# Optimization experiments

Hardware: AMD Instinct MI355X
Metric: run time of the kernel (lower is better)

Reference implementation:

```python
import jax, jax.numpy as jnp
import numpy as np

B, T, HD = 256, 512, 256
NREAL, NCAT, NCLS, ESZ = 8, 4, 10, 8
FEAT = NREAL + NCAT * NCLS          # 48 input feature dim
EMB = NREAL + NCAT * ESZ            # 40 = sum(embedding_size)
NEG_SLOPE = 0.1


def setup_inputs():
    key = jax.random.key(0)
    ks = jax.random.split(key, 18)
    g = lambda i, shape: (jax.random.normal(ks[i], shape, jnp.float32) * 0.05)
    return dict(
        x0=jax.random.normal(ks[0], (B, T, FEAT), jnp.float32),
        emb_w=g(1, (NCAT, NCLS, ESZ)),
        w1=g(2, (EMB, HD)), b1=g(3, (HD,)),
        w2=g(4, (HD, HD)), b2=g(5, (HD,)),
        wi_f=g(6, (HD, 4 * HD)), bi_f=g(7, (4 * HD,)),
        wh_f=g(8, (HD, 4 * HD)), bh_f=g(9, (4 * HD,)),
        wi_r=g(10, (HD, 4 * HD)), bi_r=g(11, (4 * HD,)),
        wh_r=g(12, (HD, 4 * HD)), bh_r=g(13, (4 * HD,)),
        w3=g(14, (2 * HD, 1)), b3=g(15, (1,)),
    )


def _lstm_final(x, wi, bi, wh, bh):
    # x: [B, T, H] -> final hidden state [B, H]; gate order F, I, A, O.
    h = wh.shape[0]
    gx = jnp.einsum('bth,hg->tbg', x, wi) + bi  # precompute i2h for all steps
    q0 = jnp.zeros((x.shape[0], h), x.dtype)
    s0 = jnp.zeros((x.shape[0], h), x.dtype)

    def step(carry, g_t):
        q, s = carry
        gates = g_t + q @ wh + bh
        f, i, a, o = jnp.split(gates, 4, axis=-1)
        s = jax.nn.sigmoid(f) * s + jax.nn.sigmoid(i) * jnp.tanh(a)
        q = jax.nn.sigmoid(o) * jnp.tanh(s)
        return (q, s), None

    (q, _), _ = jax.lax.scan(step, (q0, s0), gx)
    return q


def reference(x0, emb_w, w1, b1, w2, b2,
              wi_f, bi_f, wh_f, bh_f, wi_r, bi_r, wh_r, bh_r, w3, b3):
    lrelu = lambda v: jnp.where(v >= 0, v, NEG_SLOPE * v)
    b, t = x0.shape[0], x0.shape[1]
    x_real = x0[..., :NREAL]
    # soft embedding of categorical one-hot blocks: [B,T,NCAT,NCLS] @ [NCAT,NCLS,ESZ]
    x_cat = x0[..., NREAL:].reshape(b, t, NCAT, NCLS)
    x_emb = jnp.einsum('btcn,cne->btce', x_cat, emb_w).reshape(b, t, NCAT * ESZ)
    x1 = jnp.concatenate([x_real, x_emb], axis=-1)
    x2 = lrelu(x1 @ w1 + b1)
    x3 = lrelu(x2 @ w2 + b2)
    q_f = _lstm_final(x3, wi_f, bi_f, wh_f, bh_f)
    q_r = _lstm_final(x3[:, ::-1, :], wi_r, bi_r, wh_r, bh_r)
    x4 = jnp.concatenate([q_f, q_r], axis=1)
    return x4 @ w3 + b3
```

## Files before the change

### kernel.cpp

```cpp
#include <hip/hip_runtime.h>


#define DI __device__ __forceinline__
typedef unsigned short u16;
typedef __attribute__((ext_vector_type(8))) __bf16 bf16x8;
typedef __attribute__((ext_vector_type(8))) short short8;
typedef __attribute__((ext_vector_type(4))) float f32x4;
typedef __attribute__((ext_vector_type(2))) unsigned int u32x2;

DI float bf2f(u16 u){ unsigned v = ((unsigned)u)<<16; float f; __builtin_memcpy(&f,&v,4); return f; }
DI u16 f2bf(float f){ unsigned u; __builtin_memcpy(&u,&f,4);
  unsigned r = (u + 0x7fffu + ((u>>16)&1u))>>16; return (u16)r; }
DI float sigf(float x){ return __builtin_amdgcn_rcpf(1.f + __builtin_amdgcn_exp2f(-1.44269504f*x)); }
DI float tanh_(float x){ return 1.f - 2.f*__builtin_amdgcn_rcpf(1.f + __builtin_amdgcn_exp2f(2.88539008f*x)); }

DI void gl_lds16(const void* g, void* lds){
  __builtin_amdgcn_global_load_lds(
    (const __attribute__((address_space(1))) unsigned int*)g,
    (__attribute__((address_space(3))) unsigned int*)lds,
    16, 0, 0);
}
DI bf16x8 ld8(const void* p){ return *(const bf16x8*)p; }

__global__ void disc_wsfail(float* out){ out[0] = 1.0e9f; }

__global__ __launch_bounds__(256) void disc_prep(
    const float* __restrict__ embw, const float* __restrict__ w1, const float* __restrict__ w2,
    const float* __restrict__ wi_f, const float* __restrict__ wi_r,
    const float* __restrict__ wh_f, const float* __restrict__ wh_r,
    const float* __restrict__ bi_f, const float* __restrict__ bh_f,
    const float* __restrict__ bi_r, const float* __restrict__ bh_r,
    u16* __restrict__ w1effT, u16* __restrict__ w2bT, u16* __restrict__ wibT,
    u16* __restrict__ whp, float* __restrict__ biasf)
{
  int bx = blockIdx.x, tid = threadIdx.x;
  if (bx < 64) {
    int i = bx*256 + tid; int n = i>>6, f = i&63;
    float v = 0.f;
    if (f < 8) v = w1[f*256 + n];
    else if (f < 48) {
      int ff = f-8, c = ff/10, cls = ff%10;
      #pragma unroll
      for (int e=0;e<8;e++) v += embw[(c*10+cls)*8 + e] * w1[(8 + c*8 + e)*256 + n];
    }
    w1effT[n*64 + f] = f2bf(v);
  } else if (bx < 320) {
    int i = (bx-64)*256 + tid; int n = i>>8, k = i&255;
    w2bT[i] = f2bf(w2[k*256 + n]);
  } else if (bx < 2368) {
    int i = (bx-320)*256 + tid; int n = i>>8, k = i&255;
    const float* wi = (n < 1024) ? wi_f : wi_r; int g = n & 1023;
    wibT[i] = f2bf(wi[k*1024 + g]);
  } else if (bx < 4416) {
    int i = (bx-2368)*256 + tid;
    int j = i&7, lane = (i>>3)&63, nt = (i>>9)&7, kt = (i>>12)&7, w = (i>>15)&7, dir = (i>>18)&1;
    int k = kt*32 + (lane>>4)*8 + j;
    int g = (nt>>1)*256 + w*32 + (nt&1)*16 + (lane&15);
    const float* wh = dir ? wh_r : wh_f;
    whp[i] = f2bf(wh[k*1024 + g]);
  } else {
    int i = (bx-4416)*256 + tid;
    if (i < 2048) { int dir = i>>10, g = i&1023;
      biasf[i] = dir ? (bi_r[g]+bh_r[g]) : (bi_f[g]+bh_f[g]); }
  }
}

__global__ __launch_bounds__(256) void disc_k1a(const float* __restrict__ x0,
    const u16* __restrict__ w1effT, const float* __restrict__ b1, u16* __restrict__ x2)
{
  __shared__ __align__(16) u16 a_lds[64*64];
  __shared__ __align__(16) u16 b_lds[256*64];
  int tid=threadIdx.x, lane=tid&63, wv=tid>>6;
  int m0 = blockIdx.x*64;
  #pragma unroll
  for (int r2=0;r2<8;r2++){
    int c = r2*256 + tid;
    gl_lds16((const char*)w1effT + (size_t)c*16, (char*)b_lds + (r2*256 + wv*64)*16);
  }
  if (tid < 128){
    int row = tid>>1, half = tid&1;
    const float* src = x0 + (size_t)(m0+row)*48 + half*24;
    u16 tmp[24];
    #pragma unroll
    for (int i=0;i<24;i++) tmp[i] = f2bf(src[i]);
    #pragma unroll
    for (int i=0;i<3;i++) *(short8*)&a_lds[row*64 + half*24 + i*8] = *(short8*)&tmp[i*8];
    if (half){ short8 z = (short8){0,0,0,0,0,0,0,0};
      *(short8*)&a_lds[row*64 + 48] = z; *(short8*)&a_lds[row*64 + 56] = z; }
  }
  asm volatile("s_waitcnt vmcnt(0)" ::: "memory");
  __syncthreads();
  bf16x8 Af0 = ld8(&a_lds[(wv*16 + (lane&15))*64 + (lane>>4)*8]);
  bf16x8 Af1 = ld8(&a_lds[(wv*16 + (lane&15))*64 + 32 + (lane>>4)*8]);
  f32x4 acc[16];
  #pragma unroll
  for (int ni=0;ni<16;ni++){
    acc[ni] = (f32x4){0.f,0.f,0.f,0.f};
    bf16x8 B0 = ld8(&b_lds[(ni*16 + (lane&15))*64 + (lane>>4)*8]);
    bf16x8 B1 = ld8(&b_lds[(ni*16 + (lane&15))*64 + 32 + (lane>>4)*8]);
    acc[ni] = __builtin_amdgcn_mfma_f32_16x16x32_bf16(Af0, B0, acc[ni], 0,0,0);
    acc[ni] = __builtin_amdgcn_mfma_f32_16x16x32_bf16(Af1, B1, acc[ni], 0,0,0);
  }
  #pragma unroll
  for (int ni=0;ni<16;ni++){
    float bb = b1[ni*16 + (lane&15)];
    #pragma unroll
    for (int r=0;r<4;r++){
      float v = acc[ni][r] + bb; v = v>=0.f ? v : 0.1f*v;
      int row = m0 + wv*16 + (lane>>4)*4 + r;
      x2[(size_t)row*256 + ni*16 + (lane&15)] = f2bf(v);
    }
  }
}

__global__ __launch_bounds__(256) void disc_k1b(const u16* __restrict__ x2,
    const u16* __restrict__ w2bT, const float* __restrict__ b2, u16* __restrict__ x3t)
{
  __shared__ __align__(16) u16 a_lds[64*64];
  __shared__ __align__(16) u16 b_lds[256*64];
  int tid=threadIdx.x, lane=tid&63, wv=tid>>6;
  int m0 = blockIdx.x*64;
  f32x4 acc[16];
  #pragma unroll
  for (int ni=0;ni<16;ni++) acc[ni] = (f32x4){0.f,0.f,0.f,0.f};
  for (int kt=0;kt<4;kt++){
    #pragma unroll
    for (int r2=0;r2<2;r2++){
      int c = r2*256 + tid, row = c>>3, cb = (c&7)*16;
      gl_lds16((const char*)x2 + (size_t)(m0+row)*512 + kt*128 + cb,
               (char*)a_lds + (r2*256 + wv*64)*16);
    }
    #pragma unroll
    for (int r2=0;r2<8;r2++){
      int c = r2*256 + tid, row = c>>3, cb = (c&7)*16;
      gl_lds16((const char*)w2bT + (size_t)row*512 + kt*128 + cb,
               (char*)b_lds + (r2*256 + wv*64)*16);
    }
    asm volatile("s_waitcnt vmcnt(0)" ::: "memory");
    __syncthreads();
    bf16x8 Af0 = ld8(&a_lds[(wv*16 + (lane&15))*64 + (lane>>4)*8]);
    bf16x8 Af1 = ld8(&a_lds[(wv*16 + (lane&15))*64 + 32 + (lane>>4)*8]);
    #pragma unroll
    for (int ni=0;ni<16;ni++){
      bf16x8 B0 = ld8(&b_lds[(ni*16 + (lane&15))*64 + (lane>>4)*8]);
      bf16x8 B1 = ld8(&b_lds[(ni*16 + (lane&15))*64 + 32 + (lane>>4)*8]);
      acc[ni] = __builtin_amdgcn_mfma_f32_16x16x32_bf16(Af0, B0, acc[ni], 0,0,0);
      acc[ni] = __builtin_amdgcn_mfma_f32_16x16x32_bf16(Af1, B1, acc[ni], 0,0,0);
    }
    __syncthreads();
  }
  #pragma unroll
  for (int ni=0;ni<16;ni++){
    float bb = b2[ni*16 + (lane&15)];
    #pragma unroll
    for (int r=0;r<4;r++){
      float v = acc[ni][r] + bb; v = v>=0.f ? v : 0.1f*v;
      int rowg = m0 + wv*16 + (lane>>4)*4 + r;
      int b = rowg>>9, t = rowg&511;
      x3t[((size_t)t*256 + b)*256 + ni*16 + (lane&15)] = f2bf(v);
    }
  }
}

__global__ __launch_bounds__(256) void disc_k1c(const u16* __restrict__ x3t,
    const u16* __restrict__ wibT, const float* __restrict__ biasf,
    u16* __restrict__ gxc, int chunk)
{
  __shared__ __align__(16) u16 a_lds[128*64];
  __shared__ __align__(16) u16 b_lds[128*64];
  int tid=threadIdx.x, lane=tid&63, wv=tid>>6;
  int id = (blockIdx.x & 7)*256 + (blockIdx.x >> 3);
  int dirn = id >> 10;
  int rem  = id & 1023;
  int tloc = rem >> 4;
  int msub = (rem >> 3) & 1;
  int nt8  = rem & 7;
  int tp    = chunk*64 + tloc;
  int tglob = dirn ? (511 - tp) : tp;
  int m0 = tglob*256 + msub*128;
  int n0 = dirn*1024 + nt8*128;
  int wm = wv>>1, wn = wv&1;
  f32x4 acc[4][4];
  #pragma unroll
  for (int mi=0;mi<4;mi++)
    #pragma unroll
    for (int ni=0;ni<4;ni++) acc[mi][ni] = (f32x4){0.f,0.f,0.f,0.f};
  for (int kt=0;kt<4;kt++){
    #pragma unroll
    for (int r2=0;r2<4;r2++){
      int c = r2*256 + tid, row = c>>3, cb = (c&7)*16;
      gl_lds16((const char*)x3t + (size_t)(m0+row)*512 + kt*128 + cb,
               (char*)a_lds + (r2*256 + wv*64)*16);
    }
    #pragma unroll
    for (int r2=0;r2<4;r2++){
      int c = r2*256 + tid, row = c>>3, cb = (c&7)*16;
      gl_lds16((const char*)wibT + (size_t)(n0+row)*512 + kt*128 + cb,
               (char*)b_lds + (r2*256 + wv*64)*16);
    }
    asm volatile("s_waitcnt vmcnt(0)" ::: "memory");
    __syncthreads();
    bf16x8 Af[4][2], Bf[4][2];
    #pragma unroll
    for (int mi=0;mi<4;mi++){
      Af[mi][0] = ld8(&a_lds[(wm*64+mi*16+(lane&15))*64 + (lane>>4)*8]);
      Af[mi][1] = ld8(&a_lds[(wm*64+mi*16+(lane&15))*64 + 32 + (lane>>4)*8]);
    }
    #pragma unroll
    for (int ni=0;ni<4;ni++){
      Bf[ni][0] = ld8(&b_lds[(wn*64+ni*16+(lane&15))*64 + (lane>>4)*8]);
      Bf[ni][1] = ld8(&b_lds[(wn*64+ni*16+(lane&15))*64 + 32 + (lane>>4)*8]);
    }
    #pragma unroll
    for (int ks=0;ks<2;ks++)
      #pragma unroll
      for (int mi=0;mi<4;mi++)
        #pragma unroll
        for (int ni=0;ni<4;ni++)
          acc[mi][ni] = __builtin_amdgcn_mfma_f32_16x16x32_bf16(Af[mi][ks], Bf[ni][ks], acc[mi][ni], 0,0,0);
    __syncthreads();
  }
  float bb[4];
  #pragma unroll
  for (int ni=0;ni<4;ni++) bb[ni] = biasf[n0 + wn*64 + ni*16 + (lane&15)];
  #pragma unroll
  for (int mi=0;mi<4;mi++){
    int bbase = msub*128 + wm*64 + mi*16;
    #pragma unroll
    for (int ni=0;ni<4;ni++){
      int g0 = (n0 + wn*64 + ni*16) & 1023;
      int gt = g0>>8, h0 = g0&255;
      int w8 = h0>>5, p = (h0>>4)&1, nt = gt*2 + p;
      size_t fb = (((((size_t)tloc*2 + dirn)*16 + (bbase>>4))*8 + w8)*8 + nt)*256;
      u32x2 v;
      v.x = (unsigned)f2bf(acc[mi][ni][0]+bb[ni]) | ((unsigned)f2bf(acc[mi][ni][1]+bb[ni])<<16);
      v.y = (unsigned)f2bf(acc[mi][ni][2]+bb[ni]) | ((unsigned)f2bf(acc[mi][ni][3]+bb[ni])<<16);
      *(u32x2*)((char*)gxc + (fb + (size_t)lane*4)*2) = v;
    }
  }
}

__global__ __launch_bounds__(512) __attribute__((amdgpu_waves_per_eu(2, 2)))
void disc_k2(const u16* __restrict__ gxc, const u16* __restrict__ whp,
             u16* __restrict__ qsave, float* __restrict__ ssave,
             float* __restrict__ qout, int chunk)
{
  __shared__ __align__(16) u16 wh_lds[65536];
  __shared__ __align__(16) u16 qbuf0[4096];
  __shared__ __align__(16) u16 qbuf1[4096];
  int tid=threadIdx.x, lane=tid&63, w=tid>>6;
  int bid=blockIdx.x, dir=bid>>4, blk=bid&15;
  int tbase = chunk*64;
  int row = lane&15, rgrp = lane>>4;

  const char* whpw = (const char*)whp + (size_t)(dir*8+w)*65536;

  #pragma unroll
  for (int i=0;i<16;i++){
    int kt=i>>1, p=i&1;
    gl_lds16(whpw + (kt*8+5+p)*1024 + lane*16, (char*)wh_lds + (w*16 + i)*1024);
  }
  bf16x8 whr[8][5];
  #pragma unroll
  for (int kt=0;kt<8;kt++)
    #pragma unroll
    for (int nt=0;nt<5;nt++)
      whr[kt][nt] = ld8(whpw + (kt*8+nt)*1024 + lane*16);

  float sst[2][4];
  if (chunk==0){
    #pragma unroll
    for (int p=0;p<2;p++)
      #pragma unroll
      for (int r=0;r<4;r++) sst[p][r]=0.f;
    *(short8*)&qbuf0[tid*8] = (short8){0,0,0,0,0,0,0,0};
  } else {
    f32x4 s0 = *(const f32x4*)&ssave[((size_t)bid*512+tid)*8];
    f32x4 s1 = *(const f32x4*)&ssave[((size_t)bid*512+tid)*8 + 4];
    sst[0][0]=s0[0]; sst[0][1]=s0[1]; sst[0][2]=s0[2]; sst[0][3]=s0[3];
    sst[1][0]=s1[0]; sst[1][1]=s1[1]; sst[1][2]=s1[2]; sst[1][3]=s1[3];
    *(short8*)&qbuf0[tid*8] = *(const short8*)&qsave[(size_t)bid*4096 + tid*8];
  }

  int aoff[8];
  #pragma unroll
  for (int kt=0;kt<8;kt++)
    aoff[kt] = ((row)*512 + ((kt*64 + rgrp*16) ^ ((lane&7)<<4))) >> 1;
  int woff[2][4];
  #pragma unroll
  for (int p=0;p<2;p++)
    #pragma unroll
    for (int r=0;r<4;r++){
      int bb = rgrp*4 + r;
      woff[p][r] = (bb*512 + ((w*64 + p*32 + row*2) ^ ((bb&7)<<4))) >> 1;
    }
  int qoutbase = dir*65536 + blk*4096 + w*32 + row;
  const char* gxb = (const char*)gxc + ((size_t)(dir*16+blk)*8 + w)*4096 + (size_t)lane*8;

  asm volatile("s_waitcnt vmcnt(0)" ::: "memory");
  __syncthreads();

#define STEP(TL, QR, QW) { \
    const int tl = (TL); \
    const char* gp = gxb + (size_t)tl*1048576; \
    u32x2 gt[8]; \
    _Pragma("unroll") for (int nt=0;nt<8;nt++) gt[nt] = *(const u32x2*)(const void*)(gp + nt*512); \
    f32x4 acc[8]; \
    _Pragma("unroll") for (int nt=0;nt<8;nt++){ \
      acc[nt][0] = bf2f((u16)(gt[nt].x));       acc[nt][1] = bf2f((u16)(gt[nt].x >> 16)); \
      acc[nt][2] = bf2f((u16)(gt[nt].y));       acc[nt][3] = bf2f((u16)(gt[nt].y >> 16)); \
    } \
    bf16x8 Afr[2], sA[2]; \
    Afr[0] = ld8(&QR[aoff[0]]); \
    sA[0]  = ld8(whpw + (0*8+7)*1024 + lane*16); \
    _Pragma("unroll") for (int kt=0;kt<8;kt++){ \
      const int cur = kt&1, nxt = (kt+1)&1; \
      if (kt<7){ \
        Afr[nxt] = ld8(&QR[aoff[kt+1]]); \
        sA[nxt]  = ld8(whpw + ((kt+1)*8+7)*1024 + lane*16); \
      } \
      bf16x8 lA = ld8((char*)wh_lds + (w*16 + kt*2+0)*1024 + lane*16); \
      bf16x8 lB = ld8((char*)wh_lds + (w*16 + kt*2+1)*1024 + lane*16); \
      acc[0] = __builtin_amdgcn_mfma_f32_16x16x32_bf16(Afr[cur], whr[kt][0], acc[0], 0,0,0); \
      acc[1] = __builtin_amdgcn_mfma_f32_16x16x32_bf16(Afr[cur], whr[kt][1], acc[1], 0,0,0); \
      acc[2] = __builtin_amdgcn_mfma_f32_16x16x32_bf16(Afr[cur], whr[kt][2], acc[2], 0,0,0); \
      acc[3] = __builtin_amdgcn_mfma_f32_16x16x32_bf16(Afr[cur], whr[kt][3], acc[3], 0,0,0); \
      acc[4] = __builtin_amdgcn_mfma_f32_16x16x32_bf16(Afr[cur], whr[kt][4], acc[4], 0,0,0); \
      acc[5] = __builtin_amdgcn_mfma_f32_16x16x32_bf16(Afr[cur], lA,         acc[5], 0,0,0); \
      acc[6] = __builtin_amdgcn_mfma_f32_16x16x32_bf16(Afr[cur], lB,         acc[6], 0,0,0); \
      acc[7] = __builtin_amdgcn_mfma_f32_16x16x32_bf16(Afr[cur], sA[cur],    acc[7], 0,0,0); \
    } \
    float qv[2][4]; \
    _Pragma("unroll") for (int p=0;p<2;p++) \
      _Pragma("unroll") for (int r=0;r<4;r++){ \
        float fg = sigf (acc[0+p][r]); \
        float ig = sigf (acc[2+p][r]); \
        float ag = tanh_(acc[4+p][r]); \
        float og = sigf (acc[6+p][r]); \
        float s = fg*sst[p][r] + ig*ag; sst[p][r] = s; \
        qv[p][r] = og*tanh_(s); \
      } \
    if (tbase + tl == 511){ \
      _Pragma("unroll") for (int p=0;p<2;p++) \
        _Pragma("unroll") for (int r=0;r<4;r++) \
          qout[qoutbase + (rgrp*4 + r)*256 + p*16] = qv[p][r]; \
    } else { \
      _Pragma("unroll") for (int p=0;p<2;p++) \
        _Pragma("unroll") for (int r=0;r<4;r++) \
          QW[woff[p][r]] = f2bf(qv[p][r]); \
    } \
    __syncthreads(); \
  }

  for (int t2=0;t2<64;t2+=2){
    STEP(t2,   qbuf0, qbuf1)
    STEP(t2+1, qbuf1, qbuf0)
  }
#undef STEP

  if (chunk < 7){
    *(short8*)&qsave[(size_t)bid*4096 + tid*8] = *(const short8*)&qbuf0[tid*8];
    f32x4 s0 = (f32x4){sst[0][0],sst[0][1],sst[0][2],sst[0][3]};
    f32x4 s1 = (f32x4){sst[1][0],sst[1][1],sst[1][2],sst[1][3]};
    *(f32x4*)&ssave[((size_t)bid*512+tid)*8]     = s0;
    *(f32x4*)&ssave[((size_t)bid*512+tid)*8 + 4] = s1;
  }
}

__global__ __launch_bounds__(256) void disc_k3(const float* __restrict__ qout,
    const float* __restrict__ w3, const float* __restrict__ b3, float* __restrict__ out)
{
  int b = threadIdx.x;
  const float* qf = qout + (size_t)b*256;
  const float* qr = qout + 65536 + (size_t)b*256;
  float acc = b3[0];
  #pragma unroll 4
  for (int h=0;h<256;h++) acc += qf[h]*w3[h] + qr[h]*w3[256+h];
  out[b] = acc;
}

extern "C" void kernel_launch(void* const* d_in, const int* in_sizes, int n_in,
                              void* d_out, int out_size, void* d_ws, size_t ws_size,
                              hipStream_t stream)
{
  const float* x0   = (const float*)d_in[0];
  const float* embw = (const float*)d_in[1];
  const float* w1   = (const float*)d_in[2];
  const float* b1   = (const float*)d_in[3];
  const float* w2   = (const float*)d_in[4];
  const float* b2   = (const float*)d_in[5];
  const float* wi_f = (const float*)d_in[6];
  const float* bi_f = (const float*)d_in[7];
  const float* wh_f = (const float*)d_in[8];
  const float* bh_f = (const float*)d_in[9];
  const float* wi_r = (const float*)d_in[10];
  const float* bi_r = (const float*)d_in[11];
  const float* wh_r = (const float*)d_in[12];
  const float* bh_r = (const float*)d_in[13];
  const float* w3   = (const float*)d_in[14];
  const float* b3   = (const float*)d_in[15];

  const size_t NEED = 137797632ull;
  if (ws_size < NEED){
    disc_wsfail<<<dim3(1), dim3(1), 0, stream>>>((float*)d_out);
    return;
  }

  char* ws = (char*)d_ws;
  u16*   x2    = (u16*)  (ws);
  u16*   gxc   = (u16*)  (ws);
  u16*   x3t   = (u16*)  (ws + 67108864ull);
  u16*   whp   = (u16*)  (ws + 134217728ull);
  u16*   w1eT  = (u16*)  (ws + 135266304ull);
  u16*   w2bT  = (u16*)  (ws + 135299072ull);
  u16*   wibT  = (u16*)  (ws + 135430144ull);
  float* biasf = (float*)(ws + 136478720ull);
  float* qout  = (float*)(ws + 136486912ull);
  u16*   qsave = (u16*)  (ws + 137011200ull);
  float* ssave = (float*)(ws + 137273344ull);

  disc_prep<<<dim3(4424), dim3(256), 0, stream>>>(embw, w1, w2, wi_f, wi_r, wh_f, wh_r,
                                                  bi_f, bh_f, bi_r, bh_r,
                                                  w1eT, w2bT, wibT, whp, biasf);
  disc_k1a<<<dim3(2048), dim3(256), 0, stream>>>(x0, w1eT, b1, x2);
  disc_k1b<<<dim3(2048), dim3(256), 0, stream>>>(x2, w2bT, b2, x3t);
  for (int c = 0; c < 8; ++c){
    disc_k1c<<<dim3(2048), dim3(256), 0, stream>>>(x3t, wibT, biasf, gxc, c);
    disc_k2 <<<dim3(32),   dim3(512), 0, stream>>>(gxc, whp, qsave, ssave, qout, c);
  }
  disc_k3<<<dim3(1), dim3(256), 0, stream>>>(qout, w3, b3, (float*)d_out);
}
```

Baseline: 1.960 ms.

## Double-buffer per-step gate inputs in LDS and keep more recurrent weights in registers

The LSTM recurrence kernel now prefetches the next timestep's precomputed input-gate tile into a second LDS buffer with async global-to-LDS loads. The current step then reads its gate inputs from LDS, so global-load latency is taken off the serial per-step critical path. One more weight column tile is also moved from LDS into registers, which halves the LDS weight footprint and the per-kt LDS reads. In exchange, register pressure rises at two waves per EU, which risks spills. Correctness also relies on the barrier at the end of each step waiting for the outstanding async loads.

```diff
diff --git a/kernel.cpp b/kernel.cpp
--- a/kernel.cpp
+++ b/kernel.cpp
@@ -245,7 +245,8 @@
              u16* __restrict__ qsave, float* __restrict__ ssave,
              float* __restrict__ qout, int chunk)
 {
-  __shared__ __align__(16) u16 wh_lds[65536];
+  __shared__ __align__(16) u16 wh_lds[32768];
+  __shared__ __align__(16) u16 gx_lds[2][16384];
   __shared__ __align__(16) u16 qbuf0[4096];
   __shared__ __align__(16) u16 qbuf1[4096];
   int tid=threadIdx.x, lane=tid&63, w=tid>>6;
@@ -254,17 +255,20 @@
   int row = lane&15, rgrp = lane>>4;
 
   const char* whpw = (const char*)whp + (size_t)(dir*8+w)*65536;
-
-  #pragma unroll
-  for (int i=0;i<16;i++){
-    int kt=i>>1, p=i&1;
-    gl_lds16(whpw + (kt*8+5+p)*1024 + lane*16, (char*)wh_lds + (w*16 + i)*1024);
-  }
-  bf16x8 whr[8][5];
+  const char* gxsrc = (const char*)gxc + ((size_t)(dir*16)+blk)*32768;
+
+  #pragma unroll
+  for (int i=0;i<8;i++)
+    gl_lds16(whpw + (i*8+6)*1024 + lane*16, (char*)wh_lds + (w*8 + i)*1024);
+  #pragma unroll
+  for (int i=0;i<4;i++)
+    gl_lds16(gxsrc + w*4096 + i*1024 + lane*16,
+             (char*)gx_lds[0] + w*4096 + i*1024 + lane*16);
+  bf16x8 whr[8][6];
   #pragma unroll
   for (int kt=0;kt<8;kt++)
     #pragma unroll
-    for (int nt=0;nt<5;nt++)
+    for (int nt=0;nt<6;nt++)
       whr[kt][nt] = ld8(whpw + (kt*8+nt)*1024 + lane*16);
 
   float sst[2][4];
@@ -295,16 +299,20 @@
       woff[p][r] = (bb*512 + ((w*64 + p*32 + row*2) ^ ((bb&7)<<4))) >> 1;
     }
   int qoutbase = dir*65536 + blk*4096 + w*32 + row;
-  const char* gxb = (const char*)gxc + ((size_t)(dir*16+blk)*8 + w)*4096 + (size_t)lane*8;
 
   asm volatile("s_waitcnt vmcnt(0)" ::: "memory");
   __syncthreads();
 
-#define STEP(TL, QR, QW) { \
+#define STEP(TL, QR, QW, CUR) { \
     const int tl = (TL); \
-    const char* gp = gxb + (size_t)tl*1048576; \
+     \
+    if (tl < 63){ const char* gs = gxsrc + (size_t)(tl+1)*1048576 + w*4096; \
+      _Pragma("unroll") for (int i=0;i<4;i++) \
+        gl_lds16(gs + i*1024 + lane*16, (char*)gx_lds[(CUR)^1] + w*4096 + i*1024 + lane*16); } \
+     \
+    const char* glp = (const char*)gx_lds[CUR] + w*4096 + (size_t)lane*8; \
     u32x2 gt[8]; \
-    _Pragma("unroll") for (int nt=0;nt<8;nt++) gt[nt] = *(const u32x2*)(const void*)(gp + nt*512); \
+    _Pragma("unroll") for (int nt=0;nt<8;nt++) gt[nt] = *(const u32x2*)(const void*)(glp + nt*512); \
     f32x4 acc[8]; \
     _Pragma("unroll") for (int nt=0;nt<8;nt++){ \
       acc[nt][0] = bf2f((u16)(gt[nt].x));       acc[nt][1] = bf2f((u16)(gt[nt].x >> 16)); \
@@ -319,15 +327,14 @@
         Afr[nxt] = ld8(&QR[aoff[kt+1]]); \
         sA[nxt]  = ld8(whpw + ((kt+1)*8+7)*1024 + lane*16); \
       } \
-      bf16x8 lA = ld8((char*)wh_lds + (w*16 + kt*2+0)*1024 + lane*16); \
-      bf16x8 lB = ld8((char*)wh_lds + (w*16 + kt*2+1)*1024 + lane*16); \
+      bf16x8 lA = ld8((char*)wh_lds + (w*8 + kt)*1024 + lane*16); \
       acc[0] = __builtin_amdgcn_mfma_f32_16x16x32_bf16(Afr[cur], whr[kt][0], acc[0], 0,0,0); \
       acc[1] = __builtin_amdgcn_mfma_f32_16x16x32_bf16(Afr[cur], whr[kt][1], acc[1], 0,0,0); \
       acc[2] = __builtin_amdgcn_mfma_f32_16x16x32_bf16(Afr[cur], whr[kt][2], acc[2], 0,0,0); \
       acc[3] = __builtin_amdgcn_mfma_f32_16x16x32_bf16(Afr[cur], whr[kt][3], acc[3], 0,0,0); \
       acc[4] = __builtin_amdgcn_mfma_f32_16x16x32_bf16(Afr[cur], whr[kt][4], acc[4], 0,0,0); \
-      acc[5] = __builtin_amdgcn_mfma_f32_16x16x32_bf16(Afr[cur], lA,         acc[5], 0,0,0); \
-      acc[6] = __builtin_amdgcn_mfma_f32_16x16x32_bf16(Afr[cur], lB,         acc[6], 0,0,0); \
+      acc[5] = __builtin_amdgcn_mfma_f32_16x16x32_bf16(Afr[cur], whr[kt][5], acc[5], 0,0,0); \
+      acc[6] = __builtin_amdgcn_mfma_f32_16x16x32_bf16(Afr[cur], lA,         acc[6], 0,0,0); \
       acc[7] = __builtin_amdgcn_mfma_f32_16x16x32_bf16(Afr[cur], sA[cur],    acc[7], 0,0,0); \
     } \
     float qv[2][4]; \
@@ -353,8 +360,8 @@
   }
 
   for (int t2=0;t2<64;t2+=2){
-    STEP(t2,   qbuf0, qbuf1)
-    STEP(t2+1, qbuf1, qbuf0)
+    STEP(t2,   qbuf0, qbuf1, ((t2)&1))
+    STEP(t2+1, qbuf1, qbuf0, ((t2+1)&1))
   }
 #undef STEP
 
```

Measured after the change: 2.815 ms. +43.6%, slower.

## Overlap next-chunk input projection with LSTM recurrence in a fused launch

Applied to the files above, without the earlier changes.

Splits the time axis into 16 chunks of 32 steps and fuses the input-gate GEMM for chunk c+1 into the same launch as the recurrent LSTM for chunk c. Extra blocks beyond the first 32 compute the next chunk's gate pre-activations into a double-buffered workspace, while the first 32 blocks run the serial recurrence. The aim is to hide the GEMM behind the latency-bound recurrence, which uses only 32 CUs, and to avoid serialising separate kernels. In exchange the launch count doubles, the GEMM blocks carry the recurrent kernel's large LDS footprint and 512-thread shape, and the recurrent blocks may compete with them for CU resources.

```diff
diff --git a/kernel.cpp b/kernel.cpp
--- a/kernel.cpp
+++ b/kernel.cpp
@@ -169,13 +169,13 @@
   __shared__ __align__(16) u16 a_lds[128*64];
   __shared__ __align__(16) u16 b_lds[128*64];
   int tid=threadIdx.x, lane=tid&63, wv=tid>>6;
-  int id = (blockIdx.x & 7)*256 + (blockIdx.x >> 3);
-  int dirn = id >> 10;
-  int rem  = id & 1023;
+  int id = (blockIdx.x & 7)*128 + (blockIdx.x >> 3);
+  int dirn = id >> 9;
+  int rem  = id & 511;
   int tloc = rem >> 4;
   int msub = (rem >> 3) & 1;
   int nt8  = rem & 7;
-  int tp    = chunk*64 + tloc;
+  int tp    = chunk*32 + tloc;
   int tglob = dirn ? (511 - tp) : tp;
   int m0 = tglob*256 + msub*128;
   int n0 = dirn*1024 + nt8*128;
@@ -241,16 +241,93 @@
 }
 
 __global__ __launch_bounds__(512) __attribute__((amdgpu_waves_per_eu(2, 2)))
-void disc_k2(const u16* __restrict__ gxc, const u16* __restrict__ whp,
-             u16* __restrict__ qsave, float* __restrict__ ssave,
-             float* __restrict__ qout, int chunk)
+void disc_fused(const u16* __restrict__ gxr, u16* __restrict__ gxw,
+                const u16* __restrict__ whp,
+                const u16* __restrict__ x3t, const u16* __restrict__ wibT,
+                const float* __restrict__ biasf,
+                u16* __restrict__ qsave, float* __restrict__ ssave,
+                float* __restrict__ qout, int chunk)
 {
   __shared__ __align__(16) u16 wh_lds[65536];
   __shared__ __align__(16) u16 qbuf0[4096];
   __shared__ __align__(16) u16 qbuf1[4096];
   int tid=threadIdx.x, lane=tid&63, w=tid>>6;
+
+  if (blockIdx.x >= 32){
+    u16* a_lds = wh_lds;
+    u16* b_lds = wh_lds + 8192;
+    int gid = (int)blockIdx.x - 32;
+    int id = (gid & 7)*128 + (gid >> 3);
+    int dirn = id >> 9;
+    int rem  = id & 511;
+    int tloc = rem >> 4;
+    int msub = (rem >> 3) & 1;
+    int nt8  = rem & 7;
+    int tp    = (chunk+1)*32 + tloc;
+    int tglob = dirn ? (511 - tp) : tp;
+    int m0 = tglob*256 + msub*128;
+    int n0 = dirn*1024 + nt8*128;
+    int wm = w>>2, wn = w&3;
+    f32x4 acc[4][2];
+    #pragma unroll
+    for (int mi=0;mi<4;mi++)
+      #pragma unroll
+      for (int ni=0;ni<2;ni++) acc[mi][ni] = (f32x4){0.f,0.f,0.f,0.f};
+    for (int kt=0;kt<4;kt++){
+      #pragma unroll
+      for (int r2=0;r2<2;r2++){
+        int c = r2*512 + tid, row = c>>3, cb = (c&7)*16;
+        gl_lds16((const char*)x3t + (size_t)(m0+row)*512 + kt*128 + cb,
+                 (char*)a_lds + (r2*512 + w*64)*16);
+        int c2 = r2*512 + tid, row2 = c2>>3, cb2 = (c2&7)*16;
+        gl_lds16((const char*)wibT + (size_t)(n0+row2)*512 + kt*128 + cb2,
+                 (char*)b_lds + (r2*512 + w*64)*16);
+      }
+      asm volatile("s_waitcnt vmcnt(0)" ::: "memory");
+      __syncthreads();
+      bf16x8 Af[4][2], Bf[2][2];
+      #pragma unroll
+      for (int mi=0;mi<4;mi++){
+        Af[mi][0] = ld8(&a_lds[(wm*64+mi*16+(lane&15))*64 + (lane>>4)*8]);
+        Af[mi][1] = ld8(&a_lds[(wm*64+mi*16+(lane&15))*64 + 32 + (lane>>4)*8]);
+      }
+      #pragma unroll
+      for (int ni=0;ni<2;ni++){
+        Bf[ni][0] = ld8(&b_lds[(wn*32+ni*16+(lane&15))*64 + (lane>>4)*8]);
+        Bf[ni][1] = ld8(&b_lds[(wn*32+ni*16+(lane&15))*64 + 32 + (lane>>4)*8]);
+      }
+      #pragma unroll
+      for (int ks=0;ks<2;ks++)
+        #pragma unroll
+        for (int mi=0;mi<4;mi++)
+          #pragma unroll
+          for (int ni=0;ni<2;ni++)
+            acc[mi][ni] = __builtin_amdgcn_mfma_f32_16x16x32_bf16(Af[mi][ks], Bf[ni][ks], acc[mi][ni], 0,0,0);
+      __syncthreads();
+    }
+    float bb[2];
+    #pragma unroll
+    for (int ni=0;ni<2;ni++) bb[ni] = biasf[n0 + wn*32 + ni*16 + (lane&15)];
+    #pragma unroll
+    for (int mi=0;mi<4;mi++){
+      int bbase = msub*128 + wm*64 + mi*16;
+      #pragma unroll
+      for (int ni=0;ni<2;ni++){
+        int g0 = (n0 + wn*32 + ni*16) & 1023;
+        int gt = g0>>8, h0 = g0&255;
+        int w8 = h0>>5, p = (h0>>4)&1, nt = gt*2 + p;
+        size_t fb = (((((size_t)tloc*2 + dirn)*16 + (bbase>>4))*8 + w8)*8 + nt)*256;
+        u32x2 v;
+        v.x = (unsigned)f2bf(acc[mi][ni][0]+bb[ni]) | ((unsigned)f2bf(acc[mi][ni][1]+bb[ni])<<16);
+        v.y = (unsigned)f2bf(acc[mi][ni][2]+bb[ni]) | ((unsigned)f2bf(acc[mi][ni][3]+bb[ni])<<16);
+        *(u32x2*)((char*)gxw + (fb + (size_t)lane*4)*2) = v;
+      }
+    }
+    return;
+  }
+
   int bid=blockIdx.x, dir=bid>>4, blk=bid&15;
-  int tbase = chunk*64;
+  int tbase = chunk*32;
   int row = lane&15, rgrp = lane>>4;
 
   const char* whpw = (const char*)whp + (size_t)(dir*8+w)*65536;
@@ -295,7 +372,7 @@
       woff[p][r] = (bb*512 + ((w*64 + p*32 + row*2) ^ ((bb&7)<<4))) >> 1;
     }
   int qoutbase = dir*65536 + blk*4096 + w*32 + row;
-  const char* gxb = (const char*)gxc + ((size_t)(dir*16+blk)*8 + w)*4096 + (size_t)lane*8;
+  const char* gxb = (const char*)gxr + ((size_t)(dir*16+blk)*8 + w)*4096 + (size_t)lane*8;
 
   asm volatile("s_waitcnt vmcnt(0)" ::: "memory");
   __syncthreads();
@@ -352,13 +429,13 @@
     __syncthreads(); \
   }
 
-  for (int t2=0;t2<64;t2+=2){
+  for (int t2=0;t2<32;t2+=2){
     STEP(t2,   qbuf0, qbuf1)
     STEP(t2+1, qbuf1, qbuf0)
   }
 #undef STEP
 
-  if (chunk < 7){
+  if (chunk < 15){
     *(short8*)&qsave[(size_t)bid*4096 + tid*8] = *(const short8*)&qbuf0[tid*8];
     f32x4 s0 = (f32x4){sst[0][0],sst[0][1],sst[0][2],sst[0][3]};
     f32x4 s1 = (f32x4){sst[1][0],sst[1][1],sst[1][2],sst[1][3]};
@@ -407,8 +484,9 @@
   }
 
   char* ws = (char*)d_ws;
+  u16*   gx0   = (u16*)  (ws);
+  u16*   gx1   = (u16*)  (ws + 33554432ull);
   u16*   x2    = (u16*)  (ws);
-  u16*   gxc   = (u16*)  (ws);
   u16*   x3t   = (u16*)  (ws + 67108864ull);
   u16*   whp   = (u16*)  (ws + 134217728ull);
   u16*   w1eT  = (u16*)  (ws + 135266304ull);
@@ -424,9 +502,13 @@
                                                   w1eT, w2bT, wibT, whp, biasf);
   disc_k1a<<<dim3(2048), dim3(256), 0, stream>>>(x0, w1eT, b1, x2);
   disc_k1b<<<dim3(2048), dim3(256), 0, stream>>>(x2, w2bT, b2, x3t);
-  for (int c = 0; c < 8; ++c){
-    disc_k1c<<<dim3(2048), dim3(256), 0, stream>>>(x3t, wibT, biasf, gxc, c);
-    disc_k2 <<<dim3(32),   dim3(512), 0, stream>>>(gxc, whp, qsave, ssave, qout, c);
+  disc_k1c<<<dim3(1024), dim3(256), 0, stream>>>(x3t, wibT, biasf, gx0, 0);
+  for (int c = 0; c < 16; ++c){
+    const u16* gr = (c & 1) ? gx1 : gx0;
+    u16*       gw = (c & 1) ? gx0 : gx1;
+    int grid = (c < 15) ? 1056 : 32;
+    disc_fused<<<dim3(grid), dim3(512), 0, stream>>>(gr, gw, whp, x3t, wibT, biasf,
+                                                     qsave, ssave, qout, c);
   }
   disc_k3<<<dim3(1), dim3(256), 0, stream>>>(qout, w3, b3, (float*)d_out);
 }
```

Result: faster. 1.832 ms (median of 3 runs) (-6.5%).
